# Kernel tuning notes

Measured on AMD Instinct MI355X. Metric: run time of the kernel, lower is better.

The kernel has to match this reference:

```python
import math
import jax, jax.numpy as jnp
import numpy as np

N_HEADS = 8
WINDOW = 4


def _get_relative_embeddings(emb, length, window):
    # emb: [1, 2*window+1, k_channels] -> [1, 2*length-1, k_channels]
    pad_length = max(length - (window + 1), 0)
    start = max(window + 1 - length, 0)
    if pad_length > 0:
        emb = jnp.pad(emb, ((0, 0), (pad_length, pad_length), (0, 0)))
    return emb[:, start:start + 2 * length - 1]


def _relative_position_to_absolute_position(x):
    # x: [b, h, l, 2l-1] -> [b, h, l, l] (skewing trick)
    b, h, l, _ = x.shape
    x = jnp.pad(x, ((0, 0), (0, 0), (0, 0), (0, 1)))
    x_flat = x.reshape(b, h, l * 2 * l)
    x_flat = jnp.pad(x_flat, ((0, 0), (0, 0), (0, l - 1)))
    return x_flat.reshape(b, h, l + 1, 2 * l - 1)[:, :, :l, l - 1:]


def _absolute_position_to_relative_position(x):
    # x: [b, h, l, l] -> [b, h, l, 2l-1]
    b, h, l, _ = x.shape
    x = jnp.pad(x, ((0, 0), (0, 0), (0, 0), (0, l - 1)))
    x_flat = x.reshape(b, h, l * l + l * (l - 1))
    x_flat = jnp.pad(x_flat, ((0, 0), (0, 0), (l, 0)))
    return x_flat.reshape(b, h, l, 2 * l)[:, :, :, 1:]


def setup_inputs() -> dict:
    key = jax.random.key(0)
    ks = jax.random.split(key, 12)
    b, t, d = 4, 1024, 512
    kc = d // N_HEADS
    s = 1.0 / math.sqrt(d)
    return {
        "x": jax.random.normal(ks[0], (b, t, d), jnp.float32),
        "c": jax.random.normal(ks[1], (b, t, d), jnp.float32),
        "wq": jax.random.normal(ks[2], (d, d), jnp.float32) * s,
        "bq": jnp.zeros((d,), jnp.float32),
        "wk": jax.random.normal(ks[3], (d, d), jnp.float32) * s,
        "bk": jnp.zeros((d,), jnp.float32),
        "wv": jax.random.normal(ks[4], (d, d), jnp.float32) * s,
        "bv": jnp.zeros((d,), jnp.float32),
        "wo": jax.random.normal(ks[5], (d, d), jnp.float32) * s,
        "bo": jnp.zeros((d,), jnp.float32),
        "emb_rel_k": jax.random.normal(ks[6], (1, 2 * WINDOW + 1, kc), jnp.float32) * kc ** -0.5,
        "emb_rel_v": jax.random.normal(ks[7], (1, 2 * WINDOW + 1, kc), jnp.float32) * kc ** -0.5,
    }


def reference(x, c, wq, bq, wk, bk, wv, bv, wo, bo, emb_rel_k, emb_rel_v):
    b, t, d = x.shape
    h = N_HEADS
    kc = d // h
    inv_sqrt = 1.0 / math.sqrt(kc)

    # 1x1 conv projections (pointwise matmul)
    q = x @ wq + bq   # [b, t, d]
    k = c @ wk + bk
    v = c @ wv + bv

    # Faithful reshape as in source: [b, t, d] -> [b, h, kc, t] -> [b, h, t, kc]
    q = q.reshape(b, h, kc, t).transpose(0, 1, 3, 2)
    k = k.reshape(b, h, kc, t).transpose(0, 1, 3, 2)
    v = v.reshape(b, h, kc, t).transpose(0, 1, 3, 2)

    scores = jnp.einsum('bhtd,bhsd->bhts', q, k) * inv_sqrt  # [b,h,t,t]

    # relative key logits
    key_rel = _get_relative_embeddings(emb_rel_k, t, WINDOW)[0]  # [2t-1, kc]
    rel_logits = jnp.einsum('bhtd,md->bhtm', q, key_rel)          # [b,h,t,2t-1]
    scores_local = _relative_position_to_absolute_position(rel_logits) * inv_sqrt
    scores = scores + scores_local

    p_attn = jax.nn.softmax(scores, axis=-1)
    output = jnp.einsum('bhts,bhsd->bhtd', p_attn, v)  # [b,h,t,kc]

    # relative value contribution
    rel_weights = _absolute_position_to_relative_position(p_attn)  # [b,h,t,2t-1]
    val_rel = _get_relative_embeddings(emb_rel_v, t, WINDOW)[0]    # [2t-1, kc]
    output = output + jnp.einsum('bhtm,md->bhtd', rel_weights, val_rel)

    # Faithful output reshape: [b,h,t,kc] -> [b,h,kc,t] -> [b,t,d]
    output = output.transpose(0, 1, 3, 2).reshape(b, t, d)
    out = output @ wo + bo
    return out
```

## Files before the change

kernel.cpp:

```cpp
#include <hip/hip_runtime.h>
#include <hip/hip_bf16.h>

#define NB 4
#define NT 1024
#define ND 512
#define NH 8
#define NKC 64

typedef __bf16 bf16x8 __attribute__((ext_vector_type(8)));
typedef float f32x4 __attribute__((ext_vector_type(4)));

__device__ __forceinline__ f32x4 MFMA(bf16x8 a, bf16x8 b, f32x4 c) {
    return __builtin_amdgcn_mfma_f32_16x16x32_bf16(a, b, c, 0, 0, 0);
}
__device__ __forceinline__ unsigned short f2bu(float v) {
    __hip_bfloat16 b = __float2bfloat16(v);
    return *(unsigned short*)&b;
}
__device__ __forceinline__ void split1(float v, unsigned short& h, unsigned short& l)
{
    __hip_bfloat16 hb = __float2bfloat16(v);
    float r = v - __bfloat162float(hb);
    __hip_bfloat16 lb = __float2bfloat16(r);
    h = *(unsigned short*)&hb;
    l = *(unsigned short*)&lb;
}
__device__ __forceinline__ void splitpack(const float4 a, const float4 b, uint4& h, uint4& l)
{
    union { unsigned short u[8]; uint4 v; } H, L;
    const float f[8] = {a.x, a.y, a.z, a.w, b.x, b.y, b.z, b.w};
    #pragma unroll
    for (int j = 0; j < 8; ++j) split1(f[j], H.u[j], L.u[j]);
    h = H.v; l = L.v;
}

__global__ __launch_bounds__(256)
void splitT_kernel(const float* __restrict__ w0, const float* __restrict__ w1,
                   const float* __restrict__ w2, const float* __restrict__ w3,
                   unsigned short* __restrict__ wT)
{
    __shared__ float tl[32][33];
    const float* w = (blockIdx.z == 0) ? w0 : (blockIdx.z == 1) ? w1
                   : (blockIdx.z == 2) ? w2 : w3;
    unsigned short* hi = wT + (size_t)blockIdx.z * 2 * (ND * ND);
    unsigned short* lo = hi + ND * ND;
    const int t = threadIdx.x;
    const int x0 = blockIdx.x * 32, y0 = blockIdx.y * 32;
    {
        const int r = t >> 3, c = (t & 7) * 4;
        const float4 v = *(const float4*)&w[(size_t)(y0 + r) * ND + x0 + c];
        tl[r][c] = v.x; tl[r][c+1] = v.y; tl[r][c+2] = v.z; tl[r][c+3] = v.w;
    }
    __syncthreads();
    {
        const int nr = t >> 3, k4 = (t & 7) * 4;
        unsigned short hh[4], ll[4];
        #pragma unroll
        for (int j = 0; j < 4; ++j) split1(tl[k4 + j][nr], hh[j], ll[j]);
        ushort4 h = make_ushort4(hh[0], hh[1], hh[2], hh[3]);
        ushort4 l = make_ushort4(ll[0], ll[1], ll[2], ll[3]);
        *(ushort4*)&hi[(size_t)(x0 + nr) * ND + y0 + k4] = h;
        *(ushort4*)&lo[(size_t)(x0 + nr) * ND + y0 + k4] = l;
    }
}

__global__ __launch_bounds__(256, 3)
void proj_mfma(const float* __restrict__ x, const float* __restrict__ cc,
               const unsigned short* __restrict__ wT,
               const float* __restrict__ bq, const float* __restrict__ bk,
               const float* __restrict__ bv,
               unsigned short* __restrict__ qh_o, unsigned short* __restrict__ ql_o,
               unsigned short* __restrict__ kh_o, unsigned short* __restrict__ vh_o)
{
    __shared__ unsigned short smem[12288];
    unsigned short* Ah = smem;
    unsigned short* Al = smem + 2048;
    unsigned short* Bh = smem + 4096;
    unsigned short* Bl = smem + 8192;
    unsigned short* Tr = smem;

    const int which = blockIdx.z;
    const float* A_g = (which == 0) ? x : cc;
    const unsigned short* Bh_g = wT + (size_t)which * 2 * (ND * ND);
    const unsigned short* Bl_g = Bh_g + ND * ND;
    const float* bias = (which == 0) ? bq : (which == 1) ? bk : bv;

    const int tid = threadIdx.x, l = tid & 63, w = tid >> 6;
    const int quad = l >> 4, lc = l & 15;
    const int wm = w & 1, wn = w >> 1;
    const int n0 = blockIdx.x * 128, m0 = blockIdx.y * 64;

    const int am = tid >> 2, ak = (tid & 3) * 8;
    const size_t aG = (size_t)(m0 + am) * ND + ak;
    const int bn = tid >> 1, bk2 = (tid & 1) * 16;
    const size_t bG = (size_t)(n0 + bn) * ND + bk2;

    float4 ra0 = *(const float4*)&A_g[aG];
    float4 ra1 = *(const float4*)&A_g[aG + 4];
    uint4 rb0 = *(const uint4*)&Bh_g[bG];
    uint4 rb1 = *(const uint4*)&Bh_g[bG + 8];
    uint4 rb2 = *(const uint4*)&Bl_g[bG];
    uint4 rb3 = *(const uint4*)&Bl_g[bG + 8];

    f32x4 acc[2][4];
    #pragma unroll
    for (int mi = 0; mi < 2; ++mi)
        #pragma unroll
        for (int ni = 0; ni < 4; ++ni) acc[mi][ni] = (f32x4){0.f, 0.f, 0.f, 0.f};

    for (int k0 = 0; k0 < ND; k0 += 32) {
        __syncthreads();
        {
            uint4 h0, l0;
            splitpack(ra0, ra1, h0, l0);
            *(uint4*)&Ah[am * 32 + ak] = h0;
            *(uint4*)&Al[am * 32 + ak] = l0;
            *(uint4*)&Bh[bn * 32 + bk2] = rb0; *(uint4*)&Bh[bn * 32 + bk2 + 8] = rb1;
            *(uint4*)&Bl[bn * 32 + bk2] = rb2; *(uint4*)&Bl[bn * 32 + bk2 + 8] = rb3;
        }
        __syncthreads();
        if (k0 + 32 < ND) {
            const size_t aN = aG + k0 + 32, bN = bG + k0 + 32;
            ra0 = *(const float4*)&A_g[aN];
            ra1 = *(const float4*)&A_g[aN + 4];
            rb0 = *(const uint4*)&Bh_g[bN];
            rb1 = *(const uint4*)&Bh_g[bN + 8];
            rb2 = *(const uint4*)&Bl_g[bN];
            rb3 = *(const uint4*)&Bl_g[bN + 8];
        }

        bf16x8 ah[2], al2[2], bh[4], bl[4];
        #pragma unroll
        for (int mi = 0; mi < 2; ++mi) {
            const int ar = (wm * 32 + mi * 16 + lc) * 32 + quad * 8;
            ah[mi] = *(const bf16x8*)&Ah[ar];
            al2[mi] = *(const bf16x8*)&Al[ar];
        }
        #pragma unroll
        for (int ni = 0; ni < 4; ++ni) {
            const int br = (wn * 64 + ni * 16 + lc) * 32 + quad * 8;
            bh[ni] = *(const bf16x8*)&Bh[br];
            bl[ni] = *(const bf16x8*)&Bl[br];
        }
        #pragma unroll
        for (int mi = 0; mi < 2; ++mi)
            #pragma unroll
            for (int ni = 0; ni < 4; ++ni) {
                acc[mi][ni] = MFMA(al2[mi], bh[ni], acc[mi][ni]);
                acc[mi][ni] = MFMA(ah[mi], bl[ni], acc[mi][ni]);
                acc[mi][ni] = MFMA(ah[mi], bh[ni], acc[mi][ni]);
            }
    }

    const int bb = m0 >> 10, tt0 = m0 & 1023;
    const int hh = tt0 >> 7, cch0 = (tt0 & 127) >> 1;
    const int bh_idx = bb * NH + hh;

    if (which == 2) {
        #pragma unroll
        for (int ni = 0; ni < 4; ++ni) {
            const int n = n0 + wn * 64 + ni * 16 + lc;
            const float bval = bias[n];
            #pragma unroll
            for (int mi = 0; mi < 2; ++mi)
                #pragma unroll
                for (int r = 0; r < 4; ++r) {
                    const int mloc = wm * 32 + mi * 16 + quad * 4 + r;
                    const int cch = cch0 + (mloc >> 1);
                    const int t = (mloc & 1) * 512 + n;
                    vh_o[(((size_t)bh_idx * 16 + (t >> 6)) * 64 + cch) * 64 + (t & 63)] =
                        f2bu(acc[mi][ni][r] + bval);
                }
        }
        return;
    }

    const int npass = (which == 0) ? 2 : 1;
    unsigned short* outp[2] = {(which == 0) ? qh_o : kh_o, ql_o};

    for (int pass = 0; pass < npass; ++pass) {
        __syncthreads();
        #pragma unroll
        for (int ni = 0; ni < 4; ++ni) {
            const int nloc = wn * 64 + ni * 16 + lc;
            const float bval = bias[n0 + nloc];
            #pragma unroll
            for (int mi = 0; mi < 2; ++mi)
                #pragma unroll
                for (int r = 0; r < 4; ++r) {
                    const int mloc = wm * 32 + mi * 16 + quad * 4 + r;
                    const float val = acc[mi][ni][r] + bval;
                    unsigned short hs, ls;
                    if (which == 0) { split1(val, hs, ls); }
                    else { hs = f2bu(val); ls = 0; }
                    Tr[((mloc & 1) * 128 + nloc) * 40 + (mloc >> 1)] =
                        (pass == 0) ? hs : ls;
                }
        }
        __syncthreads();
        {
            const int t = (tid >> 7) * 512 + n0 + (tid & 127);
            const size_t oa = ((size_t)bh_idx * NT + t) * NKC + cch0;
            const uint4 v0 = *(const uint4*)&Tr[tid * 40];
            const uint4 v1 = *(const uint4*)&Tr[tid * 40 + 8];
            const uint4 v2 = *(const uint4*)&Tr[tid * 40 + 16];
            const uint4 v3 = *(const uint4*)&Tr[tid * 40 + 24];
            *(uint4*)&outp[pass][oa]      = v0;
            *(uint4*)&outp[pass][oa + 8]  = v1;
            *(uint4*)&outp[pass][oa + 16] = v2;
            *(uint4*)&outp[pass][oa + 24] = v3;
        }
    }
}

__global__ __launch_bounds__(256, 4)
void outproj_mfma(const unsigned short* __restrict__ a_g,
                  const unsigned short* __restrict__ wTh,
                  const float* __restrict__ bo, float* __restrict__ out)
{
    __shared__ unsigned short As[64 * 32], Bh[64 * 32], Bl[64 * 32];
    const unsigned short* Bl_g = wTh + ND * ND;
    const int tid = threadIdx.x, l = tid & 63, w = tid >> 6;
    const int quad = l >> 4, lc = l & 15;
    const int wm = w & 1, wn = w >> 1;
    const int n0 = blockIdx.x * 64, m0 = blockIdx.y * 64;

    const int sm = tid >> 2, sk = (tid & 3) * 8;
    const size_t aG = (size_t)(m0 + sm) * ND + sk;
    const size_t bG = (size_t)(n0 + sm) * ND + sk;

    uint4 ra  = *(const uint4*)&a_g[aG];
    uint4 rbh = *(const uint4*)&wTh[bG];
    uint4 rbl = *(const uint4*)&Bl_g[bG];

    f32x4 acc[2][2];
    #pragma unroll
    for (int mi = 0; mi < 2; ++mi)
        #pragma unroll
        for (int ni = 0; ni < 2; ++ni) acc[mi][ni] = (f32x4){0.f, 0.f, 0.f, 0.f};

    for (int k0 = 0; k0 < ND; k0 += 32) {
        __syncthreads();
        *(uint4*)&As[sm * 32 + sk] = ra;
        *(uint4*)&Bh[sm * 32 + sk] = rbh;
        *(uint4*)&Bl[sm * 32 + sk] = rbl;
        __syncthreads();
        if (k0 + 32 < ND) {
            ra  = *(const uint4*)&a_g[aG + k0 + 32];
            rbh = *(const uint4*)&wTh[bG + k0 + 32];
            rbl = *(const uint4*)&Bl_g[bG + k0 + 32];
        }
        bf16x8 ab[2], bhf[2], blf[2];
        #pragma unroll
        for (int mi = 0; mi < 2; ++mi)
            ab[mi] = *(const bf16x8*)&As[(wm * 32 + mi * 16 + lc) * 32 + quad * 8];
        #pragma unroll
        for (int ni = 0; ni < 2; ++ni) {
            const int br = (wn * 32 + ni * 16 + lc) * 32 + quad * 8;
            bhf[ni] = *(const bf16x8*)&Bh[br];
            blf[ni] = *(const bf16x8*)&Bl[br];
        }
        #pragma unroll
        for (int mi = 0; mi < 2; ++mi)
            #pragma unroll
            for (int ni = 0; ni < 2; ++ni) {
                acc[mi][ni] = MFMA(ab[mi], bhf[ni], acc[mi][ni]);
                acc[mi][ni] = MFMA(ab[mi], blf[ni], acc[mi][ni]);
            }
    }

    #pragma unroll
    for (int ni = 0; ni < 2; ++ni) {
        const int n = n0 + wn * 32 + ni * 16 + lc;
        const float bval = bo[n];
        #pragma unroll
        for (int mi = 0; mi < 2; ++mi)
            #pragma unroll
            for (int r = 0; r < 4; ++r) {
                const int m = m0 + wm * 32 + mi * 16 + quad * 4 + r;
                out[(size_t)m * ND + n] = acc[mi][ni][r] + bval;
            }
    }
}

__global__ __launch_bounds__(256, 4)
void attn_mfma(const unsigned short* __restrict__ qh_g, const unsigned short* __restrict__ ql_g,
               const unsigned short* __restrict__ kh_g,
               const unsigned short* __restrict__ vh_g,
               const float* __restrict__ embk, const float* __restrict__ embv,
               float* __restrict__ O0, float* __restrict__ O1,
               float* __restrict__ l0_g, float* __restrict__ l1_g)
{
    __shared__ unsigned short smem[19456];
    unsigned short* KsH = smem;
    unsigned short* Vt  = smem + 4608;
    unsigned short* Ps  = smem + 11264;
    float* bandv = (float*)(smem + 17920);
    unsigned short* EkH = smem + 11264;
    unsigned short* EkL = EkH + 1152;

    const int tid = threadIdx.x, l = tid & 63, w = tid >> 6;
    const int quad = l >> 4, lc = l & 15;
    const int q0 = (blockIdx.x >> 1) * 64;
    const int sh = blockIdx.x & 1;
    const int sBeg = sh * 512;
    const int hh = blockIdx.y, bb = blockIdx.z;
    const int bh = bb * NH + hh;
    const size_t qkBase = (size_t)bh * NT * NKC;
    const size_t vtBase = (size_t)bh * (16 * 64 * 64);
    float* Op = sh ? O1 : O0;
    float* lp = sh ? l1_g : l0_g;

    const int srow = tid >> 2, sseg = (tid & 3) * 16;
    uint4 pk0, pk1, pv0, pv1;
    {
        const size_t ka = qkBase + (size_t)(sBeg + srow) * NKC + sseg;
        const size_t va = vtBase + (size_t)(sBeg >> 6) * 4096 + srow * 64 + sseg;
        pk0 = *(const uint4*)&kh_g[ka];
        pk1 = *(const uint4*)&kh_g[ka + 8];
        pv0 = *(const uint4*)&vh_g[va];
        pv1 = *(const uint4*)&vh_g[va + 8];
    }

    for (int idx = tid; idx < 16 * 72; idx += 256) {
        const int d = idx / 72, kc = idx - d * 72;
        const float v = (d < 9 && kc < 64) ? embk[d * 64 + kc] : 0.f;
        unsigned short hs, ls;
        split1(v, hs, ls);
        EkH[idx] = hs;
        EkL[idx] = ls;
    }
    for (int idx = tid; idx < 64 * 40; idx += 256) {
        const int c = idx / 40, col = 64 + (idx - c * 40);
        const int d = col - 64;
        Vt[c * 104 + col] = f2bu((d < 9) ? embv[d * 64 + c] : 0.f);
    }
    __syncthreads();

    bf16x8 qh[2], ql[2];
    {
        const int qg = q0 + w * 16 + lc;
        const size_t qa = qkBase + (size_t)qg * NKC + quad * 8;
        qh[0] = *(const bf16x8*)&qh_g[qa];
        qh[1] = *(const bf16x8*)&qh_g[qa + 32];
        ql[0] = *(const bf16x8*)&ql_g[qa];
        ql[1] = *(const bf16x8*)&ql_g[qa + 32];
    }

    {
        f32x4 accB = (f32x4){0.f, 0.f, 0.f, 0.f};
        #pragma unroll
        for (int kk = 0; kk < 2; ++kk) {
            const bf16x8 ebh = *(const bf16x8*)&EkH[lc * 72 + kk * 32 + quad * 8];
            const bf16x8 ebl = *(const bf16x8*)&EkL[lc * 72 + kk * 32 + quad * 8];
            accB = MFMA(ql[kk], ebh, accB);
            accB = MFMA(qh[kk], ebl, accB);
            accB = MFMA(qh[kk], ebh, accB);
        }
        __syncthreads();
        if (lc <= 8) {
            #pragma unroll
            for (int r = 0; r < 4; ++r)
                bandv[(w * 16 + quad * 4 + r) * 12 + lc] = accB[r];
        }
    }
    unsigned short* P = Ps + w * 1664;
    {
        const int zr = l >> 2, zc = 80 + (l & 3) * 4;
        *(ushort4*)&P[zr * 104 + zc] = make_ushort4(0, 0, 0, 0);
    }

    f32x4 O[4];
    #pragma unroll
    for (int ci = 0; ci < 4; ++ci) O[ci] = (f32x4){0.f, 0.f, 0.f, 0.f};
    float l_run[4] = {0.f, 0.f, 0.f, 0.f};

    for (int s0 = sBeg; s0 < sBeg + 512; s0 += 64) {
        __syncthreads();
        {
            *(uint4*)&KsH[srow * 72 + sseg]      = pk0;
            *(uint4*)&KsH[srow * 72 + sseg + 8]  = pk1;
            *(uint4*)&Vt[srow * 104 + sseg]      = pv0;
            *(uint4*)&Vt[srow * 104 + sseg + 8]  = pv1;
        }
        __syncthreads();
        if (s0 + 64 < sBeg + 512) {
            const size_t ka = qkBase + (size_t)(s0 + 64 + srow) * NKC + sseg;
            const size_t va = vtBase + (size_t)((s0 + 64) >> 6) * 4096 + srow * 64 + sseg;
            pk0 = *(const uint4*)&kh_g[ka];
            pk1 = *(const uint4*)&kh_g[ka + 8];
            pv0 = *(const uint4*)&vh_g[va];
            pv1 = *(const uint4*)&vh_g[va + 8];
        }

        f32x4 S[4];
        #pragma unroll
        for (int ni = 0; ni < 4; ++ni) {
            f32x4 a = (f32x4){0.f, 0.f, 0.f, 0.f};
            #pragma unroll
            for (int kk = 0; kk < 2; ++kk) {
                const bf16x8 kb = *(const bf16x8*)&KsH[(ni * 16 + lc) * 72 + kk * 32 + quad * 8];
                a = MFMA(ql[kk], kb, a);
                a = MFMA(qh[kk], kb, a);
            }
            S[ni] = a;
        }

        #pragma unroll
        for (int ni = 0; ni < 4; ++ni)
            #pragma unroll
            for (int r = 0; r < 4; ++r) {
                const int ql64 = w * 16 + quad * 4 + r;
                const int dp4 = (s0 + ni * 16 + lc) - (q0 + ql64) + 4;
                float sv = S[ni][r];
                if (dp4 >= 0 && dp4 <= 8) sv += bandv[ql64 * 12 + dp4];
                S[ni][r] = __expf(sv * 0.125f);
            }
        #pragma unroll
        for (int r = 0; r < 4; ++r)
            l_run[r] += S[0][r] + S[1][r] + S[2][r] + S[3][r];

        {
            const int zr = l >> 2, zc = 64 + (l & 3) * 4;
            *(ushort4*)&P[zr * 104 + zc] = make_ushort4(0, 0, 0, 0);
        }
        #pragma unroll
        for (int ni = 0; ni < 4; ++ni)
            #pragma unroll
            for (int r = 0; r < 4; ++r) {
                const int prow = quad * 4 + r;
                const unsigned short pb = f2bu(S[ni][r]);
                P[prow * 104 + ni * 16 + lc] = pb;
                const int dp4 = (s0 + ni * 16 + lc) - (q0 + w * 16 + prow) + 4;
                if (dp4 >= 0 && dp4 <= 8) P[prow * 104 + 64 + dp4] = pb;
            }

        #pragma unroll
        for (int ks = 0; ks < 3; ++ks) {
            const bf16x8 pa = *(const bf16x8*)&P[lc * 104 + ks * 32 + quad * 8];
            #pragma unroll
            for (int ci = 0; ci < 4; ++ci) {
                const bf16x8 vb = *(const bf16x8*)&Vt[(ci * 16 + lc) * 104 + ks * 32 + quad * 8];
                O[ci] = MFMA(pa, vb, O[ci]);
            }
        }
    }

    #pragma unroll
    for (int r = 0; r < 4; ++r) {
        float v = l_run[r];
        v += __shfl_xor(v, 1); v += __shfl_xor(v, 2);
        v += __shfl_xor(v, 4); v += __shfl_xor(v, 8);
        l_run[r] = v;
    }
    const int qg0 = q0 + w * 16 + quad * 4;
    if (lc == 0) {
        #pragma unroll
        for (int r = 0; r < 4; ++r)
            lp[(size_t)bh * NT + qg0 + r] = l_run[r];
    }
    #pragma unroll
    for (int ci = 0; ci < 4; ++ci) {
        const int c = ci * 16 + lc;
        *(f32x4*)&Op[((size_t)bh * 64 + c) * NT + qg0] = O[ci];
    }
}

__global__ __launch_bounds__(256)
void combine_kernel(const float* __restrict__ O0, const float* __restrict__ O1,
                    const float* __restrict__ l0_g, const float* __restrict__ l1_g,
                    unsigned short* __restrict__ ath)
{
    const int q0 = blockIdx.x * 64, hh = blockIdx.y, bb = blockIdx.z;
    const int bh = bb * NH + hh;
    const int tid = threadIdx.x;
    __shared__ float linv[64];
    if (tid < 64)
        linv[tid] = 1.f / (l0_g[(size_t)bh * NT + q0 + tid] +
                           l1_g[(size_t)bh * NT + q0 + tid]);
    __syncthreads();

    const int c = tid >> 2, qq = (tid & 3) * 16;
    const size_t ib = ((size_t)bh * 64 + c) * NT + q0 + qq;
    union { unsigned short u[16]; uint4 v[2]; } out;
    #pragma unroll
    for (int j = 0; j < 16; j += 4) {
        const f32x4 a = *(const f32x4*)&O0[ib + j];
        const f32x4 b = *(const f32x4*)&O1[ib + j];
        #pragma unroll
        for (int r = 0; r < 4; ++r)
            out.u[j + r] = f2bu((a[r] + b[r]) * linv[qq + j + r]);
    }
    const int row = hh * 128 + 2 * c + (q0 >> 9);
    const size_t oa = ((size_t)bb * NT + row) * ND + (q0 & 511) + qq;
    *(uint4*)&ath[oa]     = out.v[0];
    *(uint4*)&ath[oa + 8] = out.v[1];
}

extern "C" void kernel_launch(void* const* d_in, const int* in_sizes, int n_in,
                              void* d_out, int out_size, void* d_ws, size_t ws_size,
                              hipStream_t stream) {
    const float* x    = (const float*)d_in[0];
    const float* c    = (const float*)d_in[1];
    const float* wq   = (const float*)d_in[2];
    const float* bq   = (const float*)d_in[3];
    const float* wk   = (const float*)d_in[4];
    const float* bk   = (const float*)d_in[5];
    const float* wv   = (const float*)d_in[6];
    const float* bv   = (const float*)d_in[7];
    const float* wo   = (const float*)d_in[8];
    const float* bo   = (const float*)d_in[9];
    const float* embk = (const float*)d_in[10];
    const float* embv = (const float*)d_in[11];

    unsigned short* u16 = (unsigned short*)d_ws;
    const size_t M = 1024 * 1024;
    unsigned short* wT  = u16;
    unsigned short* qh  = u16 + 2 * M;
    unsigned short* ql  = u16 + 4 * M;
    unsigned short* kh  = u16 + 6 * M;
    unsigned short* vh  = u16 + 8 * M;
    unsigned short* ath = u16 + 10 * M;
    float* fbase = (float*)(u16 + 12 * M);
    float* O0   = fbase;
    float* O1   = fbase + 2 * M;
    float* l0_g = fbase + 4 * M;
    float* l1_g = l0_g + 32768;

    splitT_kernel<<<dim3(16, 16, 4), 256, 0, stream>>>(wq, wk, wv, wo, wT);

    proj_mfma<<<dim3(4, 64, 3), 256, 0, stream>>>(x, c, wT, bq, bk, bv,
                                                  qh, ql, kh, vh);

    attn_mfma<<<dim3(32, 8, 4), 256, 0, stream>>>(qh, ql, kh, vh,
                                                  embk, embv, O0, O1, l0_g, l1_g);

    combine_kernel<<<dim3(16, 8, 4), 256, 0, stream>>>(O0, O1, l0_g, l1_g, ath);

    outproj_mfma<<<dim3(8, 64), 256, 0, stream>>>(ath,
                                                  wT + (size_t)3 * 2 * ND * ND,
                                                  bo, (float*)d_out);
}
```

Measured before the change: 162.7 us.

## Merge split-key attention halves into one 512-thread block, drop combine kernel

```diff
diff --git a/kernel.cpp b/kernel.cpp
--- a/kernel.cpp
+++ b/kernel.cpp
@@ -283,35 +283,37 @@
     }
 }
 
-__global__ __launch_bounds__(256, 4)
+__global__ __launch_bounds__(512, 4)
 void attn_mfma(const unsigned short* __restrict__ qh_g, const unsigned short* __restrict__ ql_g,
                const unsigned short* __restrict__ kh_g,
                const unsigned short* __restrict__ vh_g,
                const float* __restrict__ embk, const float* __restrict__ embv,
-               float* __restrict__ O0, float* __restrict__ O1,
-               float* __restrict__ l0_g, float* __restrict__ l1_g)
+               unsigned short* __restrict__ ath)
 {
-    __shared__ unsigned short smem[19456];
+    __shared__ unsigned short smem[37376];
     unsigned short* KsH = smem;
-    unsigned short* Vt  = smem + 4608;
-    unsigned short* Ps  = smem + 11264;
-    float* bandv = (float*)(smem + 17920);
-    unsigned short* EkH = smem + 11264;
+    unsigned short* Vt  = smem + 9216;
+    unsigned short* Ps  = smem + 22528;
+    float* bandv = (float*)(smem + 35840);
+    unsigned short* EkH = smem + 22528;
     unsigned short* EkL = EkH + 1152;
 
     const int tid = threadIdx.x, l = tid & 63, w = tid >> 6;
     const int quad = l >> 4, lc = l & 15;
-    const int q0 = (blockIdx.x >> 1) * 64;
-    const int sh = blockIdx.x & 1;
-    const int sBeg = sh * 512;
+    const int g = w & 3;
+    const int h = w >> 2;
+    const int q0 = blockIdx.x * 64;
+    const int sBeg = h * 512;
     const int hh = blockIdx.y, bb = blockIdx.z;
     const int bh = bb * NH + hh;
     const size_t qkBase = (size_t)bh * NT * NKC;
     const size_t vtBase = (size_t)bh * (16 * 64 * 64);
-    float* Op = sh ? O1 : O0;
-    float* lp = sh ? l1_g : l0_g;
-
-    const int srow = tid >> 2, sseg = (tid & 3) * 16;
+
+    unsigned short* KsHg = KsH + h * 4608;
+    unsigned short* Vtg  = Vt  + h * 6656;
+
+    const int tl = tid & 255;
+    const int srow = tl >> 2, sseg = (tl & 3) * 16;
     uint4 pk0, pk1, pv0, pv1;
     {
         const size_t ka = qkBase + (size_t)(sBeg + srow) * NKC + sseg;
@@ -322,7 +324,7 @@
         pv1 = *(const uint4*)&vh_g[va + 8];
     }
 
-    for (int idx = tid; idx < 16 * 72; idx += 256) {
+    for (int idx = tid; idx < 16 * 72; idx += 512) {
         const int d = idx / 72, kc = idx - d * 72;
         const float v = (d < 9 && kc < 64) ? embk[d * 64 + kc] : 0.f;
         unsigned short hs, ls;
@@ -330,16 +332,16 @@
         EkH[idx] = hs;
         EkL[idx] = ls;
     }
-    for (int idx = tid; idx < 64 * 40; idx += 256) {
-        const int c = idx / 40, col = 64 + (idx - c * 40);
-        const int d = col - 64;
-        Vt[c * 104 + col] = f2bu((d < 9) ? embv[d * 64 + c] : 0.f);
+    for (int idx = tid; idx < 2 * 64 * 40; idx += 512) {
+        const int g2 = idx / 2560, rem = idx - g2 * 2560;
+        const int c = rem / 40, d = rem - c * 40;
+        Vt[g2 * 6656 + c * 104 + 64 + d] = f2bu((d < 9) ? embv[d * 64 + c] : 0.f);
     }
     __syncthreads();
 
     bf16x8 qh[2], ql[2];
     {
-        const int qg = q0 + w * 16 + lc;
+        const int qg = q0 + g * 16 + lc;
         const size_t qa = qkBase + (size_t)qg * NKC + quad * 8;
         qh[0] = *(const bf16x8*)&qh_g[qa];
         qh[1] = *(const bf16x8*)&qh_g[qa + 32];
@@ -358,10 +360,10 @@
             accB = MFMA(qh[kk], ebh, accB);
         }
         __syncthreads();
-        if (lc <= 8) {
+        if (h == 0 && lc <= 8) {
             #pragma unroll
             for (int r = 0; r < 4; ++r)
-                bandv[(w * 16 + quad * 4 + r) * 12 + lc] = accB[r];
+                bandv[(g * 16 + quad * 4 + r) * 12 + lc] = accB[r];
         }
     }
     unsigned short* P = Ps + w * 1664;
@@ -378,10 +380,10 @@
     for (int s0 = sBeg; s0 < sBeg + 512; s0 += 64) {
         __syncthreads();
         {
-            *(uint4*)&KsH[srow * 72 + sseg]      = pk0;
-            *(uint4*)&KsH[srow * 72 + sseg + 8]  = pk1;
-            *(uint4*)&Vt[srow * 104 + sseg]      = pv0;
-            *(uint4*)&Vt[srow * 104 + sseg + 8]  = pv1;
+            *(uint4*)&KsHg[srow * 72 + sseg]      = pk0;
+            *(uint4*)&KsHg[srow * 72 + sseg + 8]  = pk1;
+            *(uint4*)&Vtg[srow * 104 + sseg]      = pv0;
+            *(uint4*)&Vtg[srow * 104 + sseg + 8]  = pv1;
         }
         __syncthreads();
         if (s0 + 64 < sBeg + 512) {
@@ -399,7 +401,7 @@
             f32x4 a = (f32x4){0.f, 0.f, 0.f, 0.f};
             #pragma unroll
             for (int kk = 0; kk < 2; ++kk) {
-                const bf16x8 kb = *(const bf16x8*)&KsH[(ni * 16 + lc) * 72 + kk * 32 + quad * 8];
+                const bf16x8 kb = *(const bf16x8*)&KsHg[(ni * 16 + lc) * 72 + kk * 32 + quad * 8];
                 a = MFMA(ql[kk], kb, a);
                 a = MFMA(qh[kk], kb, a);
             }
@@ -410,7 +412,7 @@
         for (int ni = 0; ni < 4; ++ni)
             #pragma unroll
             for (int r = 0; r < 4; ++r) {
-                const int ql64 = w * 16 + quad * 4 + r;
+                const int ql64 = g * 16 + quad * 4 + r;
                 const int dp4 = (s0 + ni * 16 + lc) - (q0 + ql64) + 4;
                 float sv = S[ni][r];
                 if (dp4 >= 0 && dp4 <= 8) sv += bandv[ql64 * 12 + dp4];
@@ -431,7 +433,7 @@
                 const int prow = quad * 4 + r;
                 const unsigned short pb = f2bu(S[ni][r]);
                 P[prow * 104 + ni * 16 + lc] = pb;
-                const int dp4 = (s0 + ni * 16 + lc) - (q0 + w * 16 + prow) + 4;
+                const int dp4 = (s0 + ni * 16 + lc) - (q0 + g * 16 + prow) + 4;
                 if (dp4 >= 0 && dp4 <= 8) P[prow * 104 + 64 + dp4] = pb;
             }
 
@@ -440,7 +442,7 @@
             const bf16x8 pa = *(const bf16x8*)&P[lc * 104 + ks * 32 + quad * 8];
             #pragma unroll
             for (int ci = 0; ci < 4; ++ci) {
-                const bf16x8 vb = *(const bf16x8*)&Vt[(ci * 16 + lc) * 104 + ks * 32 + quad * 8];
+                const bf16x8 vb = *(const bf16x8*)&Vtg[(ci * 16 + lc) * 104 + ks * 32 + quad * 8];
                 O[ci] = MFMA(pa, vb, O[ci]);
             }
         }
@@ -453,48 +455,42 @@
         v += __shfl_xor(v, 4); v += __shfl_xor(v, 8);
         l_run[r] = v;
     }
-    const int qg0 = q0 + w * 16 + quad * 4;
-    if (lc == 0) {
+
+    __syncthreads();
+    float* Oex = (float*)smem;
+    float* l1s = bandv;
+    const int qloc0 = g * 16 + quad * 4;
+
+    if (h == 1) {
+        #pragma unroll
+        for (int ci = 0; ci < 4; ++ci)
+            #pragma unroll
+            for (int r = 0; r < 4; ++r)
+                Oex[(qloc0 + r) * 64 + ci * 16 + lc] = O[ci][r];
+        if (lc == 0) {
+            #pragma unroll
+            for (int r = 0; r < 4; ++r)
+                l1s[qloc0 + r] = l_run[r];
+        }
+    }
+    __syncthreads();
+    if (h == 0) {
+        float linv[4];
         #pragma unroll
         for (int r = 0; r < 4; ++r)
-            lp[(size_t)bh * NT + qg0 + r] = l_run[r];
-    }
-    #pragma unroll
-    for (int ci = 0; ci < 4; ++ci) {
-        const int c = ci * 16 + lc;
-        *(f32x4*)&Op[((size_t)bh * 64 + c) * NT + qg0] = O[ci];
-    }
-}
-
-__global__ __launch_bounds__(256)
-void combine_kernel(const float* __restrict__ O0, const float* __restrict__ O1,
-                    const float* __restrict__ l0_g, const float* __restrict__ l1_g,
-                    unsigned short* __restrict__ ath)
-{
-    const int q0 = blockIdx.x * 64, hh = blockIdx.y, bb = blockIdx.z;
-    const int bh = bb * NH + hh;
-    const int tid = threadIdx.x;
-    __shared__ float linv[64];
-    if (tid < 64)
-        linv[tid] = 1.f / (l0_g[(size_t)bh * NT + q0 + tid] +
-                           l1_g[(size_t)bh * NT + q0 + tid]);
-    __syncthreads();
-
-    const int c = tid >> 2, qq = (tid & 3) * 16;
-    const size_t ib = ((size_t)bh * 64 + c) * NT + q0 + qq;
-    union { unsigned short u[16]; uint4 v[2]; } out;
-    #pragma unroll
-    for (int j = 0; j < 16; j += 4) {
-        const f32x4 a = *(const f32x4*)&O0[ib + j];
-        const f32x4 b = *(const f32x4*)&O1[ib + j];
-        #pragma unroll
-        for (int r = 0; r < 4; ++r)
-            out.u[j + r] = f2bu((a[r] + b[r]) * linv[qq + j + r]);
-    }
-    const int row = hh * 128 + 2 * c + (q0 >> 9);
-    const size_t oa = ((size_t)bb * NT + row) * ND + (q0 & 511) + qq;
-    *(uint4*)&ath[oa]     = out.v[0];
-    *(uint4*)&ath[oa + 8] = out.v[1];
+            linv[r] = 1.f / (l_run[r] + l1s[qloc0 + r]);
+        #pragma unroll
+        for (int ci = 0; ci < 4; ++ci) {
+            const int c = ci * 16 + lc;
+            const int row = hh * 128 + 2 * c + (q0 >> 9);
+            unsigned short o[4];
+            #pragma unroll
+            for (int r = 0; r < 4; ++r)
+                o[r] = f2bu((O[ci][r] + Oex[(qloc0 + r) * 64 + c]) * linv[r]);
+            *(ushort4*)&ath[((size_t)bb * NT + row) * ND + (q0 & 511) + qloc0] =
+                make_ushort4(o[0], o[1], o[2], o[3]);
+        }
+    }
 }
 
 extern "C" void kernel_launch(void* const* d_in, const int* in_sizes, int n_in,
@@ -521,21 +517,14 @@
     unsigned short* kh  = u16 + 6 * M;
     unsigned short* vh  = u16 + 8 * M;
     unsigned short* ath = u16 + 10 * M;
-    float* fbase = (float*)(u16 + 12 * M);
-    float* O0   = fbase;
-    float* O1   = fbase + 2 * M;
-    float* l0_g = fbase + 4 * M;
-    float* l1_g = l0_g + 32768;
 
     splitT_kernel<<<dim3(16, 16, 4), 256, 0, stream>>>(wq, wk, wv, wo, wT);
 
     proj_mfma<<<dim3(4, 64, 3), 256, 0, stream>>>(x, c, wT, bq, bk, bv,
                                                   qh, ql, kh, vh);
 
-    attn_mfma<<<dim3(32, 8, 4), 256, 0, stream>>>(qh, ql, kh, vh,
-                                                  embk, embv, O0, O1, l0_g, l1_g);
-
-    combine_kernel<<<dim3(16, 8, 4), 256, 0, stream>>>(O0, O1, l0_g, l1_g, ath);
+    attn_mfma<<<dim3(16, 8, 4), 512, 0, stream>>>(qh, ql, kh, vh,
+                                                  embk, embv, ath);
 
     outproj_mfma<<<dim3(8, 64), 256, 0, stream>>>(ath,
                                                   wT + (size_t)3 * 2 * ND * ND,
```

Measured after the change: 158.6 us. 2.5% less time.
